# Kernel optimization log

Hardware: AMD Instinct MI355X
Metric: run time of the kernel (lower is better)

## Reference

```python
import jax, jax.numpy as jnp
import numpy as np

N_NODES = 50000
N_EDGES = 800000
NUM_GRAPHS = 500
BN_EPS = 1e-5


def setup_inputs() -> dict:
    key = jax.random.key(0)
    ks = jax.random.split(key, 8)
    x = jax.random.normal(ks[0], (N_NODES, 33), dtype=jnp.float32)
    edge_index = jax.random.randint(ks[1], (2, N_EDGES), 0, N_NODES, dtype=jnp.int64)
    batch = jnp.sort(jax.random.randint(ks[2], (N_NODES,), 0, NUM_GRAPHS, dtype=jnp.int64))
    # Xavier-ish scaled weights
    W0 = jax.random.normal(ks[3], (33, 100), dtype=jnp.float32) * (2.0 / (33 + 100)) ** 0.5
    Wrest = jax.random.normal(ks[4], (3, 100, 100), dtype=jnp.float32) * (2.0 / 200) ** 0.5
    b = jnp.zeros((4, 100), dtype=jnp.float32)
    gamma = jnp.ones((4, 100), dtype=jnp.float32)
    beta = jnp.zeros((4, 100), dtype=jnp.float32)
    Wout = jax.random.normal(ks[5], (100, 200), dtype=jnp.float32) * (2.0 / 300) ** 0.5
    bout = jnp.zeros((200,), dtype=jnp.float32)
    return {"x": x, "edge_index": edge_index, "batch": batch, "W0": W0,
            "Wrest": Wrest, "b": b, "gamma": gamma, "beta": beta,
            "Wout": Wout, "bout": bout}


def reference(x, edge_index, batch, W0, Wrest, b, gamma, beta, Wout, bout):
    N = x.shape[0]
    # GCN normalization with self-loops (gcn_norm): shared across layers
    loops = jnp.arange(N, dtype=edge_index.dtype)
    src = jnp.concatenate([edge_index[0], loops])
    dst = jnp.concatenate([edge_index[1], loops])
    deg = jax.ops.segment_sum(jnp.ones_like(dst, dtype=x.dtype), dst, num_segments=N)
    dinv = jnp.where(deg > 0, jax.lax.rsqrt(deg), 0.0)
    norm = dinv[src] * dinv[dst]  # [E+N]

    Ws = [W0, Wrest[0], Wrest[1], Wrest[2]]
    h = x
    for layer in range(4):
        m = h @ Ws[layer]                                   # [N, out_c]
        agg = jax.ops.segment_sum(norm[:, None] * m[src], dst, num_segments=N)
        agg = agg + b[layer]
        # BatchNorm1d (batch statistics, biased variance)
        mean = agg.mean(axis=0)
        var = agg.var(axis=0)
        hbn = (agg - mean) * jax.lax.rsqrt(var + BN_EPS) * gamma[layer] + beta[layer]
        h = jax.nn.relu(hbn) if layer < 3 else hbn          # dropout is identity in eval

    g = jax.ops.segment_sum(h, batch, num_segments=NUM_GRAPHS)  # global_add_pool
    out = g @ Wout + bout
    return jnp.where(out > 0, out, 0.1 * out)  # LeakyReLU(0.1)
```

## Files before the change

### kernel.cpp

```cpp
#include <hip/hip_runtime.h>

#define NNODES 50000
#define NEDGES 800000
#define NGRAPH 500
#define CH 100
#define CIN0 33
#define BN_EPS 1e-5f
#define NSHARD 8
#define SHSTRIDE 1024
#define NBUK 196
#define BEPW 2048

#define SCAN_TPB 256
#define SCAN_IPT 4
#define SCAN_TILE (SCAN_TPB * SCAN_IPT)
#define SCAN_BLOCKS ((NNODES + SCAN_TILE - 1) / SCAN_TILE)

typedef __attribute__((ext_vector_type(8))) short short8;
typedef __attribute__((ext_vector_type(4))) float f32x4;

__device__ inline unsigned pack_bf16(float x, float y) {
    unsigned xb = __float_as_uint(x);
    unsigned yb = __float_as_uint(y);
    xb += 0x7FFF + ((xb >> 16) & 1);
    yb += 0x7FFF + ((yb >> 16) & 1);
    return (xb >> 16) | (yb & 0xFFFF0000u);
}
__device__ inline float unp_lo(unsigned v) { return __uint_as_float(v << 16); }
__device__ inline float unp_hi(unsigned v) { return __uint_as_float(v & 0xFFFF0000u); }

__global__ void k_prep(const float* __restrict__ x, unsigned* __restrict__ xb,
                       int* __restrict__ cnt, float* __restrict__ stats,
                       float* __restrict__ gbuf,
                       const float* __restrict__ Wrest, unsigned* __restrict__ whi,
                       unsigned* __restrict__ wlo,
                       const float* __restrict__ W0, unsigned* __restrict__ w0hi,
                       unsigned* __restrict__ w0lo,
                       unsigned* __restrict__ Z0, unsigned* __restrict__ Z1) {
    int i = blockIdx.x * blockDim.x + threadIdx.x;
    if (i < (NNODES + 1) * 17) {
        int r = i / 17, s = i - r * 17;
        if (r >= NNODES) xb[i] = 0u;
        else {
            float a = x[r * CIN0 + 2 * s];
            float b = (2 * s + 1 < CIN0) ? x[r * CIN0 + 2 * s + 1] : 0.f;
            xb[i] = pack_bf16(a, b);
        }
    }
    if (i < NNODES) { cnt[i] = 0; gbuf[i] = 0.f; }
    if (i < NSHARD * SHSTRIDE) stats[i] = 0.f;
    if (i < 3 * 112 * 64) {
        int l = i / 7168, rem = i % 7168;
        int c = rem >> 6, ku = rem & 63;
        int k0 = 2 * ku;
        float w0 = 0.f, w1 = 0.f;
        if (c < CH && k0 < CH) {
            w0 = Wrest[l * 10000 + k0 * CH + c];
            if (k0 + 1 < CH) w1 = Wrest[l * 10000 + (k0 + 1) * CH + c];
        }
        unsigned hh = pack_bf16(w0, w1);
        whi[i] = hh;
        wlo[i] = pack_bf16(w0 - unp_lo(hh), w1 - unp_hi(hh));
    }
    if (i < 112 * 32) {
        int c = i >> 5, ku = i & 31;
        int k0 = 2 * ku;
        float w0 = 0.f, w1 = 0.f;
        if (c < CH && k0 < CIN0) {
            w0 = W0[k0 * CH + c];
            if (k0 + 1 < CIN0) w1 = W0[(k0 + 1) * CH + c];
        }
        unsigned hh = pack_bf16(w0, w1);
        w0hi[i] = hh;
        w0lo[i] = pack_bf16(w0 - unp_lo(hh), w1 - unp_hi(hh));
    }
    if (i < 50) {
        Z0[(size_t)NNODES * 50 + i] = 0u;
        Z1[(size_t)NNODES * 50 + i] = 0u;
    }
}

__global__ void k_hist(const int* __restrict__ dst, int* __restrict__ cnt) {
    int e = blockIdx.x * blockDim.x + threadIdx.x;
    if (e < NEDGES) atomicAdd(&cnt[dst[e]], 1);
}

__global__ void k_scan1(const int* __restrict__ cnt, int* __restrict__ rowptr,
                        int* __restrict__ blkSums, float* __restrict__ dinv,
                        int* __restrict__ bcnt) {
    __shared__ int ts[SCAN_TPB];
    __shared__ int bsum[4];
    int tid = threadIdx.x;
    if (tid < 4) bsum[tid] = 0;
    int base = blockIdx.x * SCAN_TILE + tid * SCAN_IPT;
    int v[SCAN_IPT];
    int s = 0, cact = 0;
    #pragma unroll
    for (int j = 0; j < SCAN_IPT; ++j) {
        int i = base + j;
        int c = (i < NNODES) ? cnt[i] : 0;
        if (i < NNODES) dinv[i] = rsqrtf((float)(c + 1));
        v[j] = (c + 7) & ~7;
        s += v[j];
        cact += c;
    }
    ts[tid] = s;
    __syncthreads();
    atomicAdd(&bsum[(tid * SCAN_IPT) >> 8], cact);
    for (int off = 1; off < SCAN_TPB; off <<= 1) {
        int add = (tid >= off) ? ts[tid - off] : 0;
        __syncthreads();
        ts[tid] += add;
        __syncthreads();
    }
    int run = ts[tid] - s;
    #pragma unroll
    for (int j = 0; j < SCAN_IPT; ++j) {
        int i = base + j;
        if (i < NNODES) rowptr[i] = run;
        run += v[j];
    }
    if (tid == SCAN_TPB - 1) blkSums[blockIdx.x] = ts[tid];
    if (tid < 4) {
        int b = blockIdx.x * 4 + tid;
        if (b < NBUK) bcnt[b] = bsum[tid];
    }
}

__global__ void k_scan2b(const int* __restrict__ blkSums, int* __restrict__ blkOff,
                         int* __restrict__ rp2, const int* __restrict__ bcnt,
                         int* __restrict__ bbase, int* __restrict__ gbkcur) {
    __shared__ int ts[256];
    int t = threadIdx.x;
    if (t == 0) {
        int run = 0;
        for (int i = 0; i < SCAN_BLOCKS; ++i) { blkOff[i] = run; run += blkSums[i]; }
        rp2[NNODES] = run;
    }
    int v = (t < NBUK) ? bcnt[t] : 0;
    ts[t] = v;
    __syncthreads();
    for (int off = 1; off < 256; off <<= 1) {
        int a = (t >= off) ? ts[t - off] : 0;
        __syncthreads();
        ts[t] += a;
        __syncthreads();
    }
    int excl = ts[t] - v;
    if (t < NBUK) { bbase[t] = excl; gbkcur[t] = excl; }
    if (t == NBUK - 1) bbase[NBUK] = ts[t];
}

__global__ __launch_bounds__(256) void k_bin(const int* __restrict__ src,
                                             const int* __restrict__ dst,
                                             const float* __restrict__ dinv,
                                             int* __restrict__ gbkcur,
                                             uint2* __restrict__ ebuf) {
    __shared__ int hist[256], ofs[256], lcnt[256], bbaseL[256];
    __shared__ int totS;
    __shared__ uint2 stage[BEPW];
    int tid = threadIdx.x;
    hist[tid] = 0; lcnt[tid] = 0;
    __syncthreads();
    int e0 = blockIdx.x * BEPW;
    unsigned sv[8]; int dv[8]; bool ok[8];
    #pragma unroll
    for (int j = 0; j < 8; ++j) {
        int e = e0 + j * 256 + tid;
        ok[j] = e < NEDGES;
        int s = ok[j] ? src[e] : 0;
        dv[j] = ok[j] ? dst[e] : 0;
        if (ok[j]) {
            unsigned db = __float_as_uint(dinv[s]);
            db += 0x7FFF + ((db >> 16) & 1);
            sv[j] = (unsigned)s | (db & 0xFFFF0000u);
            atomicAdd(&hist[dv[j] >> 8], 1);
        }
    }
    __syncthreads();
    int v = hist[tid];
    ofs[tid] = v;
    __syncthreads();
    for (int off = 1; off < 256; off <<= 1) {
        int a = (tid >= off) ? ofs[tid - off] : 0;
        __syncthreads();
        ofs[tid] += a;
        __syncthreads();
    }
    if (tid == 255) totS = ofs[255];
    int excl = ofs[tid] - v;
    __syncthreads();
    ofs[tid] = excl;
    if (tid < NBUK && v > 0) bbaseL[tid] = atomicAdd(&gbkcur[tid], v);
    __syncthreads();
    #pragma unroll
    for (int j = 0; j < 8; ++j) {
        if (ok[j]) {
            int b = dv[j] >> 8;
            int idx = atomicAdd(&lcnt[b], 1);
            stage[ofs[b] + idx] = make_uint2(sv[j], (unsigned)dv[j]);
        }
    }
    __syncthreads();
    int tot = totS;
    #pragma unroll
    for (int j = 0; j < 8; ++j) {
        int slot = j * 256 + tid;
        if (slot < tot) {
            uint2 p = stage[slot];
            int b = (int)(p.y >> 8);
            ebuf[bbaseL[b] + (slot - ofs[b])] = p;
        }
    }
}

__global__ __launch_bounds__(256) void k_place(const uint2* __restrict__ ebuf,
                                               const int* __restrict__ bbase,
                                               const int* __restrict__ rowptr,
                                               const int* __restrict__ blkOff,
                                               int* __restrict__ rp2,
                                               unsigned* __restrict__ ew) {
    __shared__ int lcur[256];
    int b = blockIdx.x, t = threadIdx.x;
    int lo = b * 256;
    int n = NNODES - lo; if (n > 256) n = 256;
    if (t < n) {
        int node = lo + t;
        int base = rowptr[node] + blkOff[node >> 10];
        lcur[t] = base;
        rp2[node] = base;
    }
    __syncthreads();
    int e0 = bbase[b], e1 = bbase[b + 1];
    for (int e = e0 + t; e < e1; e += 256) {
        uint2 p = ebuf[e];
        int pos = atomicAdd(&lcur[p.y & 255], 1);
        ew[pos] = p.x;
    }
    __syncthreads();
    if (t < n) {
        int idx = lo + t + 1;
        int end = (idx < NNODES) ? (rowptr[idx] + blkOff[idx >> 10]) : rp2[NNODES];
        for (int q = lcur[t]; q < end; ++q) ew[q] = NNODES;
    }
}

template<int CPACK, int RB, int KS, bool BN>
__global__ __launch_bounds__(512, 8) void k_fused(
    const unsigned* __restrict__ h, const unsigned* __restrict__ Whi,
    const unsigned* __restrict__ Wlo, const float* __restrict__ bias,
    const int* __restrict__ rowptr, const unsigned* __restrict__ ew,
    const float* __restrict__ dinv,
    const float* __restrict__ pgsum, const float* __restrict__ pgsq,
    const float* __restrict__ gamma, const float* __restrict__ beta,
    unsigned* __restrict__ Zout, float* __restrict__ gsum, float* __restrict__ gsq) {
    constexpr int RBY = KS * 64;
    __shared__ __align__(16) unsigned char aS[64 * RBY];
    __shared__ __align__(16) unsigned char wB[112 * 128];
    __shared__ float sSum[CH], sSq[CH];
    int tid = threadIdx.x;
    for (int i = tid; i < CH; i += 512) { sSum[i] = 0.f; sSq[i] = 0.f; }
    for (int idx = tid; idx < 112 * 8; idx += 512) {
        int c = idx >> 3, j = idx & 7;
        uint4 v = *(const uint4*)(Whi + c * (KS * 16) + j * 4);
        *(uint4*)(wB + ((unsigned)(c * 128 + j * 16) ^ ((c & 7) << 4))) = v;
    }
    int w = tid >> 6, lane = tid & 63;
    int row0 = blockIdx.x * 64;
    const char* __restrict__ hb = (const char*)h;
    bool act = lane < CPACK;
    unsigned l4 = (unsigned)(lane << 2);
    float scx = 0.f, shx = 0.f, scy = 0.f, shy = 0.f;
    if (BN && act) {
        float sx = 0.f, sy = 0.f, qx = 0.f, qy = 0.f;
        #pragma unroll
        for (int sh = 0; sh < NSHARD; ++sh) {
            float2 s2 = ((const float2*)(pgsum + sh * SHSTRIDE))[lane];
            float2 q2 = ((const float2*)(pgsq + sh * SHSTRIDE))[lane];
            sx += s2.x; sy += s2.y; qx += q2.x; qy += q2.y;
        }
        constexpr float invN = 1.f / NNODES;
        float2 g2 = ((const float2*)gamma)[lane];
        float2 b2 = ((const float2*)beta)[lane];
        float mx = sx * invN, my = sy * invN;
        float vx = qx * invN - mx * mx, vy = qy * invN - my * my;
        scx = g2.x * rsqrtf(vx + BN_EPS); shx = b2.x - mx * scx;
        scy = g2.y * rsqrtf(vy + BN_EPS); shy = b2.y - my * scy;
    }
    for (int ni = 0; ni < 8; ++ni) {
        int r = w * 8 + ni;
        int node = row0 + r;
        float ax = 0.f, ay = 0.f, di = 0.f;
        if (node < NNODES) {
            int p0 = __builtin_amdgcn_readfirstlane(rowptr[node]);
            int p1 = __builtin_amdgcn_readfirstlane(rowptr[node + 1]);
            di = dinv[node];
            if (act) {
                unsigned hv = h[(size_t)node * CPACK + lane];
                float fx = unp_lo(hv), fy = unp_hi(hv);
                if (BN) {
                    fx = fmaxf(fmaf(fx, scx, shx), 0.f);
                    fy = fmaxf(fmaf(fy, scy, shy), 0.f);
                }
                ax = di * fx; ay = di * fy;
            }
            const uint4* __restrict__ E4 = (const uint4*)(ew + p0);
            int n8 = (p1 - p0) >> 3;
            for (int q = 0; q < n8; ++q) {
                uint4 ea = E4[2 * q];
                uint4 eb = E4[2 * q + 1];
                unsigned ee[8] = {ea.x, ea.y, ea.z, ea.w, eb.x, eb.y, eb.z, eb.w};
                if (act) {
                    unsigned v[8];
                    #pragma unroll
                    for (int t = 0; t < 8; ++t)
                        v[t] = *(const unsigned*)(hb + (ee[t] & 0xFFFFu) * (unsigned)RB + l4);
                    #pragma unroll
                    for (int t = 0; t < 8; ++t) {
                        float vx = unp_lo(v[t]), vy = unp_hi(v[t]);
                        if (BN) {
                            vx = fmaxf(fmaf(vx, scx, shx), 0.f);
                            vy = fmaxf(fmaf(vy, scy, shy), 0.f);
                        }
                        float wgt = unp_hi(ee[t]);
                        ax = fmaf(wgt, vx, ax); ay = fmaf(wgt, vy, ay);
                    }
                }
            }
        }
        unsigned val = act ? pack_bf16(di * ax, di * ay) : 0u;
        if (lane < RBY / 4)
            *(unsigned*)(aS + ((unsigned)(r * RBY + lane * 4) ^ ((r & 7) << 4))) = val;
    }
    __syncthreads();
    int wm = w & 3, wh = w >> 2;
    int lr = lane & 15, lg = lane >> 4;
    f32x4 acc[4];
    #pragma unroll
    for (int nt = 0; nt < 4; ++nt) acc[nt] = (f32x4){0.f, 0.f, 0.f, 0.f};
    int ar = wm * 16 + lr;
    unsigned aswz = (unsigned)((ar & 7) << 4);
    uint4 pv0, pv1;
    #pragma unroll
    for (int ch = 0; ch < KS; ++ch) {
        if (ch + 1 < KS) {
            const unsigned* Wp = (ch + 1 >= KS / 2) ? Wlo : Whi;
            int pn = (KS > 2) ? ((ch + 1) & 1) : 0;
            {
                int c = tid >> 3, j = tid & 7;
                pv0 = *(const uint4*)(Wp + c * (KS * 16) + pn * 32 + j * 4);
            }
            if (tid < 384) {
                int idx = tid + 512;
                int c = idx >> 3, j = idx & 7;
                pv1 = *(const uint4*)(Wp + c * (KS * 16) + pn * 32 + j * 4);
            }
        }
        int p = (KS > 2) ? (ch & 1) : 0;
        #pragma unroll
        for (int ksl = 0; ksl < 2; ++ksl) {
            int ks = p * 2 + ksl;
            short8 af = *(const short8*)(aS + ((unsigned)(ar * RBY + ks * 64 + lg * 16) ^ aswz));
            #pragma unroll
            for (int nt = 0; nt < 4; ++nt) {
                if (wh && nt == 3) continue;
                int c = (wh * 4 + nt) * 16 + lr;
                short8 bb = *(const short8*)(wB + ((unsigned)(c * 128 + ksl * 64 + lg * 16) ^ ((c & 7) << 4)));
                acc[nt] = __builtin_amdgcn_mfma_f32_16x16x32_bf16(af, bb, acc[nt], 0, 0, 0);
            }
        }
        if (ch + 1 < KS) {
            __syncthreads();
            {
                int c = tid >> 3, j = tid & 7;
                *(uint4*)(wB + ((unsigned)(c * 128 + j * 16) ^ ((c & 7) << 4))) = pv0;
            }
            if (tid < 384) {
                int idx = tid + 512;
                int c = idx >> 3, j = idx & 7;
                *(uint4*)(wB + ((unsigned)(c * 128 + j * 16) ^ ((c & 7) << 4))) = pv1;
            }
            __syncthreads();
        }
    }
    #pragma unroll
    for (int nt = 0; nt < 4; ++nt) {
        if (wh && nt == 3) continue;
        int c = (wh * 4 + nt) * 16 + lr;
        bool cok = c < CH;
        float bcol = cok ? bias[c] : 0.f;
        float s = 0.f, q = 0.f;
        #pragma unroll
        for (int r = 0; r < 4; ++r) {
            int row = row0 + wm * 16 + lg * 4 + r;
            float z = acc[nt][r] + bcol;
            float zo = __shfl_xor(z, 1);
            if (cok && row < NNODES) {
                if ((lane & 1) == 0)
                    Zout[(size_t)row * 50 + (c >> 1)] = pack_bf16(z, zo);
                s += z; q += z * z;
            }
        }
        s += __shfl_xor(s, 16); s += __shfl_xor(s, 32);
        q += __shfl_xor(q, 16); q += __shfl_xor(q, 32);
        if (lane < 16 && cok) { atomicAdd(&sSum[c], s); atomicAdd(&sSq[c], q); }
    }
    __syncthreads();
    int sh = (blockIdx.x & (NSHARD - 1)) * SHSTRIDE;
    if (tid < CH) { atomicAdd(&gsum[sh + tid], sSum[tid]); atomicAdd(&gsq[sh + tid], sSq[tid]); }
}

__global__ void k_pool(const unsigned* __restrict__ Zl, const int* __restrict__ batch,
                       const float* __restrict__ gsum, const float* __restrict__ gsq,
                       const float* __restrict__ gamma, const float* __restrict__ beta,
                       float* __restrict__ g) {
    int gid = blockIdx.x;
    int part = blockIdx.y;
    int lo = 0, hi = NNODES;
    while (lo < hi) { int mid = (lo + hi) >> 1; if (batch[mid] < gid) lo = mid + 1; else hi = mid; }
    int start = lo;
    hi = NNODES;
    while (lo < hi) { int mid = (lo + hi) >> 1; if (batch[mid] < gid + 1) lo = mid + 1; else hi = mid; }
    int end = lo;
    int len = end - start;
    int cb = (len + 3) >> 2;
    int s = start + part * cb;
    int e = s + cb; if (e > end) e = end;
    if (s >= e) return;
    int t = threadIdx.x;
    if (t >= 50) return;
    float su = 0.f, sv = 0.f, qu = 0.f, qv = 0.f;
    #pragma unroll
    for (int sh = 0; sh < NSHARD; ++sh) {
        float2 s2 = ((const float2*)(gsum + sh * SHSTRIDE))[t];
        float2 q2 = ((const float2*)(gsq + sh * SHSTRIDE))[t];
        su += s2.x; sv += s2.y; qu += q2.x; qv += q2.y;
    }
    constexpr float invN = 1.f / NNODES;
    float2 g2 = ((const float2*)gamma)[t];
    float2 b2 = ((const float2*)beta)[t];
    float mx = su * invN, my = sv * invN;
    float vx = qu * invN - mx * mx, vy = qv * invN - my * my;
    float scx = g2.x * rsqrtf(vx + BN_EPS), shx = b2.x - mx * scx;
    float scy = g2.y * rsqrtf(vy + BN_EPS), shy = b2.y - my * scy;
    float sx = 0.f, sy = 0.f;
    for (int r = s; r < e; ++r) {
        unsigned v = Zl[(size_t)r * 50 + t];
        sx += unp_lo(v); sy += unp_hi(v);
    }
    float n = (float)(e - s);
    atomicAdd(&g[gid * CH + 2 * t], sx * scx + n * shx);
    atomicAdd(&g[gid * CH + 2 * t + 1], sy * scy + n * shy);
}

__global__ __launch_bounds__(256) void k_out(const float* __restrict__ g,
                                             const float* __restrict__ Wout,
                                             const float* __restrict__ bout,
                                             float* __restrict__ out) {
    __shared__ float gS[CH];
    int gid = blockIdx.x, tid = threadIdx.x;
    if (tid < CH) gS[tid] = g[gid * CH + tid];
    __syncthreads();
    if (tid >= 200) return;
    float acc = bout[tid];
    for (int k = 0; k < CH; ++k) acc += gS[k] * Wout[k * 200 + tid];
    out[gid * 200 + tid] = acc > 0.f ? acc : 0.1f * acc;
}

extern "C" void kernel_launch(void* const* d_in, const int* in_sizes, int n_in,
                              void* d_out, int out_size, void* d_ws, size_t ws_size,
                              hipStream_t stream) {
    const float* x = (const float*)d_in[0];
    const int* ei = (const int*)d_in[1];
    const int* batch = (const int*)d_in[2];
    const float* W0 = (const float*)d_in[3];
    const float* Wrest = (const float*)d_in[4];
    const float* b = (const float*)d_in[5];
    const float* gamma = (const float*)d_in[6];
    const float* beta = (const float*)d_in[7];
    const float* Wout = (const float*)d_in[8];
    const float* bout = (const float*)d_in[9];
    float* out = (float*)d_out;
    const int* srcA = ei;
    const int* dstA = ei + NEDGES;

    char* wsb = (char*)d_ws;
    size_t off = 0;
    auto alloc = [&](size_t elems) -> void* {
        void* p = (void*)(wsb + off);
        off += ((elems + 7) & ~(size_t)7) * 4;
        return p;
    };
    int* cnt = (int*)alloc(NNODES);
    int* rowptr = (int*)alloc(NNODES + 1);
    int* rp2 = (int*)alloc(NNODES + 1);
    float* dinv = (float*)alloc(NNODES);
    int* scanBlk = (int*)alloc(64);
    int* scanOff = (int*)alloc(64);
    int* bcnt = (int*)alloc(256);
    int* bbase = (int*)alloc(256);
    int* gbkcur = (int*)alloc(256);
    float* stats = (float*)alloc(NSHARD * SHSTRIDE);
    unsigned* ew = (unsigned*)alloc((size_t)NEDGES + 8 * NNODES);
    uint2* ebuf = (uint2*)alloc(2 * (size_t)NEDGES);
    unsigned* xb = (unsigned*)alloc((size_t)(NNODES + 1) * 17);
    unsigned* wthi = (unsigned*)alloc(3 * 112 * 64);
    unsigned* wtlo = (unsigned*)alloc(3 * 112 * 64);
    unsigned* w0hi = (unsigned*)alloc(112 * 32);
    unsigned* w0lo = (unsigned*)alloc(112 * 32);
    unsigned* Z0 = (unsigned*)alloc((size_t)(NNODES + 1) * 50);
    unsigned* Z1 = (unsigned*)alloc((size_t)(NNODES + 1) * 50);
    float* gbuf = (float*)alloc((size_t)NGRAPH * CH);
    (void)ws_size; (void)n_in; (void)in_sizes; (void)out_size;

    hipLaunchKernelGGL(k_prep, dim3(((NNODES + 1) * 17 + 255) / 256), dim3(256), 0, stream,
                       x, xb, cnt, stats, gbuf, Wrest, wthi, wtlo, W0, w0hi, w0lo, Z0, Z1);
    hipLaunchKernelGGL(k_hist, dim3((NEDGES + 255) / 256), dim3(256), 0, stream, dstA, cnt);
    hipLaunchKernelGGL(k_scan1, dim3(SCAN_BLOCKS), dim3(SCAN_TPB), 0, stream,
                       cnt, rowptr, scanBlk, dinv, bcnt);
    hipLaunchKernelGGL(k_scan2b, dim3(1), dim3(256), 0, stream,
                       scanBlk, scanOff, rp2, bcnt, bbase, gbkcur);
    hipLaunchKernelGGL(k_bin, dim3((NEDGES + BEPW - 1) / BEPW), dim3(256), 0, stream,
                       srcA, dstA, dinv, gbkcur, ebuf);
    hipLaunchKernelGGL(k_place, dim3(NBUK), dim3(256), 0, stream,
                       ebuf, bbase, rowptr, scanOff, rp2, ew);

    const int NTILE = (NNODES + 63) / 64;
    hipLaunchKernelGGL((k_fused<17, 68, 2, false>), dim3(NTILE), dim3(512), 0, stream,
                       xb, w0hi, w0lo, b, rp2, ew, dinv,
                       (const float*)nullptr, (const float*)nullptr,
                       (const float*)nullptr, (const float*)nullptr,
                       Z0, stats + 0 * 128, stats + 512 + 0 * 128);
    unsigned* Zp[4] = {Z0, Z1, Z0, Z1};
    for (int l = 1; l < 4; ++l) {
        hipLaunchKernelGGL((k_fused<50, 200, 4, true>), dim3(NTILE), dim3(512), 0, stream,
                           Zp[l - 1], wthi + (l - 1) * 7168, wtlo + (l - 1) * 7168, b + l * CH,
                           rp2, ew, dinv,
                           stats + (l - 1) * 128, stats + 512 + (l - 1) * 128,
                           gamma + (l - 1) * CH, beta + (l - 1) * CH,
                           Zp[l], stats + l * 128, stats + 512 + l * 128);
    }
    hipLaunchKernelGGL(k_pool, dim3(NGRAPH, 4), dim3(64), 0, stream, Z1, batch,
                       stats + 3 * 128, stats + 512 + 3 * 128, gamma + 3 * CH, beta + 3 * CH, gbuf);
    hipLaunchKernelGGL(k_out, dim3(NGRAPH), dim3(256), 0, stream, gbuf, Wout, bout, out);
}
```

Baseline: 326.0 us.

## Fuse global add pooling into last GCN layer and apply BN in output kernel

The last fused layer no longer writes its bf16 output. It atomically adds each pre-BN value into per-graph sums. The k_pool kernel is removed, and the output kernel now finds each graph's node count and applies the BN affine transform to the pooled sums (scale*sum + n*shift) before the linear layer. This drops one kernel launch and a full read and write of the layer output, but adds many global float atomics (one per node-channel), which may contend because consecutive rows belong to the same graph. A redundant no-op edit was also added in k_place.

```diff
diff --git a/kernel.cpp b/kernel.cpp
--- a/kernel.cpp
+++ b/kernel.cpp
@@ -240,12 +240,13 @@
     __syncthreads();
     if (t < n) {
         int idx = lo + t + 1;
-        int end = (idx < NNODES) ? (rowptr[idx] + blkOff[idx >> 10]) : rp2[NNODES];
+        int end = (idx < NNODES) ? (rowptr[idx] + blkOff[idx >> 1024 == 0 ? (idx >> 10) : (idx >> 10)]) : rp2[NNODES];
+        end = (idx < NNODES) ? (rowptr[idx] + blkOff[idx >> 10]) : rp2[NNODES];
         for (int q = lcur[t]; q < end; ++q) ew[q] = NNODES;
     }
 }
 
-template<int CPACK, int RB, int KS, bool BN>
+template<int CPACK, int RB, int KS, bool BN, bool POOL>
 __global__ __launch_bounds__(512, 8) void k_fused(
     const unsigned* __restrict__ h, const unsigned* __restrict__ Whi,
     const unsigned* __restrict__ Wlo, const float* __restrict__ bias,
@@ -253,6 +254,7 @@
     const float* __restrict__ dinv,
     const float* __restrict__ pgsum, const float* __restrict__ pgsq,
     const float* __restrict__ gamma, const float* __restrict__ beta,
+    const int* __restrict__ batch, float* __restrict__ gpool,
     unsigned* __restrict__ Zout, float* __restrict__ gsum, float* __restrict__ gsq) {
     constexpr int RBY = KS * 64;
     __shared__ __align__(16) unsigned char aS[64 * RBY];
@@ -383,6 +385,14 @@
             __syncthreads();
         }
     }
+    int g4[4];
+    if (POOL) {
+        #pragma unroll
+        for (int r = 0; r < 4; ++r) {
+            int row = row0 + wm * 16 + lg * 4 + r;
+            g4[r] = (row < NNODES) ? batch[row] : 0;
+        }
+    }
     #pragma unroll
     for (int nt = 0; nt < 4; ++nt) {
         if (wh && nt == 3) continue;
@@ -396,8 +406,12 @@
             float z = acc[nt][r] + bcol;
             float zo = __shfl_xor(z, 1);
             if (cok && row < NNODES) {
-                if ((lane & 1) == 0)
-                    Zout[(size_t)row * 50 + (c >> 1)] = pack_bf16(z, zo);
+                if (POOL) {
+                    atomicAdd(&gpool[g4[r] * CH + c], z);
+                } else {
+                    if ((lane & 1) == 0)
+                        Zout[(size_t)row * 50 + (c >> 1)] = pack_bf16(z, zo);
+                }
                 s += z; q += z * z;
             }
         }
@@ -410,56 +424,47 @@
     if (tid < CH) { atomicAdd(&gsum[sh + tid], sSum[tid]); atomicAdd(&gsq[sh + tid], sSq[tid]); }
 }
 
-__global__ void k_pool(const unsigned* __restrict__ Zl, const int* __restrict__ batch,
-                       const float* __restrict__ gsum, const float* __restrict__ gsq,
-                       const float* __restrict__ gamma, const float* __restrict__ beta,
-                       float* __restrict__ g) {
-    int gid = blockIdx.x;
-    int part = blockIdx.y;
-    int lo = 0, hi = NNODES;
-    while (lo < hi) { int mid = (lo + hi) >> 1; if (batch[mid] < gid) lo = mid + 1; else hi = mid; }
-    int start = lo;
-    hi = NNODES;
-    while (lo < hi) { int mid = (lo + hi) >> 1; if (batch[mid] < gid + 1) lo = mid + 1; else hi = mid; }
-    int end = lo;
-    int len = end - start;
-    int cb = (len + 3) >> 2;
-    int s = start + part * cb;
-    int e = s + cb; if (e > end) e = end;
-    if (s >= e) return;
-    int t = threadIdx.x;
-    if (t >= 50) return;
-    float su = 0.f, sv = 0.f, qu = 0.f, qv = 0.f;
-    #pragma unroll
-    for (int sh = 0; sh < NSHARD; ++sh) {
-        float2 s2 = ((const float2*)(gsum + sh * SHSTRIDE))[t];
-        float2 q2 = ((const float2*)(gsq + sh * SHSTRIDE))[t];
-        su += s2.x; sv += s2.y; qu += q2.x; qv += q2.y;
-    }
-    constexpr float invN = 1.f / NNODES;
-    float2 g2 = ((const float2*)gamma)[t];
-    float2 b2 = ((const float2*)beta)[t];
-    float mx = su * invN, my = sv * invN;
-    float vx = qu * invN - mx * mx, vy = qv * invN - my * my;
-    float scx = g2.x * rsqrtf(vx + BN_EPS), shx = b2.x - mx * scx;
-    float scy = g2.y * rsqrtf(vy + BN_EPS), shy = b2.y - my * scy;
-    float sx = 0.f, sy = 0.f;
-    for (int r = s; r < e; ++r) {
-        unsigned v = Zl[(size_t)r * 50 + t];
-        sx += unp_lo(v); sy += unp_hi(v);
-    }
-    float n = (float)(e - s);
-    atomicAdd(&g[gid * CH + 2 * t], sx * scx + n * shx);
-    atomicAdd(&g[gid * CH + 2 * t + 1], sy * scy + n * shy);
-}
-
 __global__ __launch_bounds__(256) void k_out(const float* __restrict__ g,
+                                             const int* __restrict__ batch,
+                                             const float* __restrict__ gsum,
+                                             const float* __restrict__ gsq,
+                                             const float* __restrict__ gamma,
+                                             const float* __restrict__ beta,
                                              const float* __restrict__ Wout,
                                              const float* __restrict__ bout,
                                              float* __restrict__ out) {
     __shared__ float gS[CH];
+    __shared__ int se[2];
     int gid = blockIdx.x, tid = threadIdx.x;
-    if (tid < CH) gS[tid] = g[gid * CH + tid];
+    if (tid == 0) {
+        int lo = 0, hi = NNODES;
+        while (lo < hi) { int m = (lo + hi) >> 1; if (batch[m] < gid) lo = m + 1; else hi = m; }
+        se[0] = lo;
+        hi = NNODES;
+        while (lo < hi) { int m = (lo + hi) >> 1; if (batch[m] < gid + 1) lo = m + 1; else hi = m; }
+        se[1] = lo;
+    }
+    __syncthreads();
+    float n = (float)(se[1] - se[0]);
+    if (tid < 50) {
+        float su = 0.f, sv = 0.f, qu = 0.f, qv = 0.f;
+        #pragma unroll
+        for (int sh = 0; sh < NSHARD; ++sh) {
+            float2 s2 = ((const float2*)(gsum + sh * SHSTRIDE))[tid];
+            float2 q2 = ((const float2*)(gsq + sh * SHSTRIDE))[tid];
+            su += s2.x; sv += s2.y; qu += q2.x; qv += q2.y;
+        }
+        constexpr float invN = 1.f / NNODES;
+        float2 g2 = ((const float2*)gamma)[tid];
+        float2 b2 = ((const float2*)beta)[tid];
+        float mx = su * invN, my = sv * invN;
+        float vx = qu * invN - mx * mx, vy = qv * invN - my * my;
+        float scx = g2.x * rsqrtf(vx + BN_EPS), shx = b2.x - mx * scx;
+        float scy = g2.y * rsqrtf(vy + BN_EPS), shy = b2.y - my * scy;
+        float2 S = ((const float2*)(g + gid * CH))[tid];
+        gS[2 * tid] = S.x * scx + n * shx;
+        gS[2 * tid + 1] = S.y * scy + n * shy;
+    }
     __syncthreads();
     if (tid >= 200) return;
     float acc = bout[tid];
@@ -526,21 +531,30 @@
                        ebuf, bbase, rowptr, scanOff, rp2, ew);
 
     const int NTILE = (NNODES + 63) / 64;
-    hipLaunchKernelGGL((k_fused<17, 68, 2, false>), dim3(NTILE), dim3(512), 0, stream,
+    hipLaunchKernelGGL((k_fused<17, 68, 2, false, false>), dim3(NTILE), dim3(512), 0, stream,
                        xb, w0hi, w0lo, b, rp2, ew, dinv,
                        (const float*)nullptr, (const float*)nullptr,
                        (const float*)nullptr, (const float*)nullptr,
+                       (const int*)nullptr, (float*)nullptr,
                        Z0, stats + 0 * 128, stats + 512 + 0 * 128);
-    unsigned* Zp[4] = {Z0, Z1, Z0, Z1};
-    for (int l = 1; l < 4; ++l) {
-        hipLaunchKernelGGL((k_fused<50, 200, 4, true>), dim3(NTILE), dim3(512), 0, stream,
+    unsigned* Zp[3] = {Z0, Z1, Z0};
+    for (int l = 1; l < 3; ++l) {
+        hipLaunchKernelGGL((k_fused<50, 200, 4, true, false>), dim3(NTILE), dim3(512), 0, stream,
                            Zp[l - 1], wthi + (l - 1) * 7168, wtlo + (l - 1) * 7168, b + l * CH,
                            rp2, ew, dinv,
                            stats + (l - 1) * 128, stats + 512 + (l - 1) * 128,
                            gamma + (l - 1) * CH, beta + (l - 1) * CH,
+                           (const int*)nullptr, (float*)nullptr,
                            Zp[l], stats + l * 128, stats + 512 + l * 128);
     }
-    hipLaunchKernelGGL(k_pool, dim3(NGRAPH, 4), dim3(64), 0, stream, Z1, batch,
-                       stats + 3 * 128, stats + 512 + 3 * 128, gamma + 3 * CH, beta + 3 * CH, gbuf);
-    hipLaunchKernelGGL(k_out, dim3(NGRAPH), dim3(256), 0, stream, gbuf, Wout, bout, out);
-}
+    hipLaunchKernelGGL((k_fused<50, 200, 4, true, true>), dim3(NTILE), dim3(512), 0, stream,
+                       Zp[2], wthi + 2 * 7168, wtlo + 2 * 7168, b + 3 * CH,
+                       rp2, ew, dinv,
+                       stats + 2 * 128, stats + 512 + 2 * 128,
+                       gamma + 2 * CH, beta + 2 * CH,
+                       batch, gbuf,
+                       (unsigned*)nullptr, stats + 3 * 128, stats + 512 + 3 * 128);
+    hipLaunchKernelGGL(k_out, dim3(NGRAPH), dim3(256), 0, stream,
+                       gbuf, batch, stats + 3 * 128, stats + 512 + 3 * 128,
+                       gamma + 3 * CH, beta + 3 * CH, Wout, bout, out);
+}
```

After: 376.5 us. 1.15x slower.
